# Performance work log

Measured on AMD Instinct MI355X. Metric: run time of the kernel, lower is better.

## Reference

```python
import jax, jax.numpy as jnp
import numpy as np

N_NODES = 50000
N_EDGES = 800000
D_IN = 128
D_HID = 256


def setup_inputs() -> dict:
    key = jax.random.key(0)
    ks = jax.random.split(key, 8)
    x = jax.random.normal(ks[0], (N_NODES, D_IN), dtype=jnp.float32)
    edge_index = jax.random.randint(ks[1], (2, N_EDGES), 0, N_NODES, dtype=jnp.int32)
    s1 = 1.0 / np.sqrt(D_IN)
    s2 = 1.0 / np.sqrt(D_HID)
    W1_l = jax.random.uniform(ks[2], (D_IN, D_HID), jnp.float32, -s1, s1)
    W1_r = jax.random.uniform(ks[3], (D_IN, D_HID), jnp.float32, -s1, s1)
    b1 = jax.random.uniform(ks[4], (D_HID,), jnp.float32, -s1, s1)
    W2_l = jax.random.uniform(ks[5], (D_HID, D_HID), jnp.float32, -s2, s2)
    W2_r = jax.random.uniform(ks[6], (D_HID, D_HID), jnp.float32, -s2, s2)
    b2 = jax.random.uniform(ks[7], (D_HID,), jnp.float32, -s2, s2)
    return {"x": x, "edge_index": edge_index,
            "W1_l": W1_l, "W1_r": W1_r, "b1": b1,
            "W2_l": W2_l, "W2_r": W2_r, "b2": b2}


def _sage_conv(x, src, dst, deg_inv, W_l, W_r, b):
    # mean-aggregate neighbor features at destination nodes, then
    # out = lin_l(mean_neighbors) + lin_r(x)  (PyG SAGEConv, mean aggr)
    msgs = x[src]                                              # [E, d]  irregular gather
    agg = jax.ops.segment_sum(msgs, dst, num_segments=x.shape[0])  # [N, d] scatter-add
    mean = agg * deg_inv[:, None]
    return mean @ W_l + x @ W_r + b


def reference(x, edge_index, W1_l, W1_r, b1, W2_l, W2_r, b2):
    src, dst = edge_index[0], edge_index[1]
    n = x.shape[0]
    deg = jax.ops.segment_sum(jnp.ones_like(dst, dtype=x.dtype), dst, num_segments=n)
    deg_inv = jnp.where(deg > 0, 1.0 / jnp.maximum(deg, 1.0), 0.0)
    h = jax.nn.relu(_sage_conv(x, src, dst, deg_inv, W1_l, W1_r, b1))
    # dropout is identity in eval mode
    out = jax.nn.relu(_sage_conv(h, src, dst, deg_inv, W2_l, W2_r, b2))
    return out
```

## Files before the change

kernel.cpp:

```cpp
#include <hip/hip_runtime.h>
#include <hip/hip_bf16.h>


#define DIN 128
#define DH  256
#define ELLW 64

typedef __attribute__((ext_vector_type(8))) short short8v;
typedef __attribute__((ext_vector_type(4))) float float4v;
typedef __attribute__((ext_vector_type(2))) float float2v;

__device__ __forceinline__ void gload_lds16(const void* g, void* l) {
    __builtin_amdgcn_global_load_lds((const __attribute__((address_space(1))) void*)g,
                                     (__attribute__((address_space(3))) void*)l, 16, 0, 0);
}
__device__ __forceinline__ float bf2f(unsigned short u) {
    union { unsigned int i; float f; } c; c.i = ((unsigned int)u) << 16; return c.f;
}
__device__ __forceinline__ unsigned short f2bf(float f) {
    union { float f; unsigned int i; } c; c.f = f;
    unsigned int lsb = (c.i >> 16) & 1u;
    return (unsigned short)((c.i + 0x7fffu + lsb) >> 16);
}
__device__ __host__ __forceinline__ int permcol(int q) {
    return ((q >> 6) << 6) + ((q & 3) << 4) + ((q >> 2) & 15);
}

__global__ void fill_ell(const int* __restrict__ src, const int* __restrict__ dst,
                         int* __restrict__ cnt, unsigned short* __restrict__ ell, int E) {
    int base = (blockIdx.x * blockDim.x + threadIdx.x) * 8;
    if (base + 7 < E) {
        int4 da = *(const int4*)(dst + base);
        int4 db = *(const int4*)(dst + base + 4);
        int4 sa = *(const int4*)(src + base);
        int4 sb = *(const int4*)(src + base + 4);
        int p0 = atomicAdd(&cnt[da.x], 1);
        int p1 = atomicAdd(&cnt[da.y], 1);
        int p2 = atomicAdd(&cnt[da.z], 1);
        int p3 = atomicAdd(&cnt[da.w], 1);
        int p4 = atomicAdd(&cnt[db.x], 1);
        int p5 = atomicAdd(&cnt[db.y], 1);
        int p6 = atomicAdd(&cnt[db.z], 1);
        int p7 = atomicAdd(&cnt[db.w], 1);
        if (p0 < ELLW) ell[(size_t)da.x * ELLW + p0] = (unsigned short)sa.x;
        if (p1 < ELLW) ell[(size_t)da.y * ELLW + p1] = (unsigned short)sa.y;
        if (p2 < ELLW) ell[(size_t)da.z * ELLW + p2] = (unsigned short)sa.z;
        if (p3 < ELLW) ell[(size_t)da.w * ELLW + p3] = (unsigned short)sa.w;
        if (p4 < ELLW) ell[(size_t)db.x * ELLW + p4] = (unsigned short)sb.x;
        if (p5 < ELLW) ell[(size_t)db.y * ELLW + p5] = (unsigned short)sb.y;
        if (p6 < ELLW) ell[(size_t)db.z * ELLW + p6] = (unsigned short)sb.z;
        if (p7 < ELLW) ell[(size_t)db.w * ELLW + p7] = (unsigned short)sb.w;
    } else {
        for (int e = base; e < E; ++e) {
            int d = dst[e];
            int p = atomicAdd(&cnt[d], 1);
            if (p < ELLW) ell[(size_t)d * ELLW + p] = (unsigned short)src[e];
        }
    }
}

__global__ void prep_weights(const float* __restrict__ W1l, const float* __restrict__ W1r,
                             const float* __restrict__ W2l, const float* __restrict__ W2r,
                             unsigned short* __restrict__ Wt1, unsigned short* __restrict__ Wt2) {
    int id = blockIdx.x * 256 + threadIdx.x;
    if (id < 256 * 256) {
        int n = id >> 8, k = id & 255;
        float v = (k < 128) ? W1l[k * 256 + n] : W1r[(k - 128) * 256 + n];
        Wt1[n * 256 + k] = f2bf(v);
    } else {
        int id2 = id - 256 * 256;
        if (id2 < 256 * 512) {
            int n = id2 >> 9, k = id2 & 511;
            float v;
            if (k < 256) v = W2l[permcol(k) * 256 + n];
            else         v = W2r[permcol(k - 256) * 256 + n];
            Wt2[n * 512 + k] = f2bf(v);
        }
    }
}

__global__ void conv_x(const float* __restrict__ x, unsigned short* __restrict__ Acat1,
                       unsigned char* __restrict__ xf8, int N) {
    int id = blockIdx.x * 256 + threadIdx.x;
    int base = id * 4;
    if (base < N * 128) {
        float4 v = *(const float4*)(x + base);
        int row = base >> 7, c = base & 127;
        ushort4 o;
        o.x = f2bf(v.x); o.y = f2bf(v.y); o.z = f2bf(v.z); o.w = f2bf(v.w);
        *(ushort4*)(Acat1 + (size_t)row * 256 + 128 + c) = o;
        int p = __builtin_amdgcn_cvt_pk_fp8_f32(v.x, v.y, 0, false);
        p = __builtin_amdgcn_cvt_pk_fp8_f32(v.z, v.w, p, true);
        *(unsigned int*)(xf8 + (size_t)row * 128 + c) = (unsigned int)p;
    }
}

template <int LANES, int RSTRB, int WSTR>
__global__ __launch_bounds__(256) void agg_fp8(const unsigned char* __restrict__ f8,
                                               const unsigned short* __restrict__ ell,
                                               const int* __restrict__ cnt,
                                               unsigned short* __restrict__ outp, int N) {
    int tid = threadIdx.x;
    constexpr int NPB = 256 / LANES;
    int node = blockIdx.x * NPB + tid / LANES;
    int lane = tid % LANES;
    if (node >= N) return;
    int cn = cnt[node];
    int dg = min(cn, ELLW);
    const unsigned short* row = ell + (size_t)node * ELLW;
    const unsigned char* fb = f8 + (size_t)lane * 16;
    float acc[16];
#pragma unroll
    for (int e = 0; e < 16; ++e) acc[e] = 0.f;
    int j = 0;
    for (; j + 8 <= dg; j += 8) {
        int s[8];
#pragma unroll
        for (int q = 0; q < 8; ++q) s[q] = row[j + q];
        int4 v[8];
#pragma unroll
        for (int q = 0; q < 8; ++q) v[q] = *(const int4*)(fb + (size_t)s[q] * RSTRB);
#pragma unroll
        for (int q = 0; q < 8; ++q) {
            int wv[4] = {v[q].x, v[q].y, v[q].z, v[q].w};
#pragma unroll
            for (int wI = 0; wI < 4; ++wI) {
                float2v lo = __builtin_amdgcn_cvt_pk_f32_fp8(wv[wI], false);
                float2v hi = __builtin_amdgcn_cvt_pk_f32_fp8(wv[wI], true);
                acc[wI * 4 + 0] += lo[0];
                acc[wI * 4 + 1] += lo[1];
                acc[wI * 4 + 2] += hi[0];
                acc[wI * 4 + 3] += hi[1];
            }
        }
    }
    for (; j < dg; ++j) {
        int s = row[j];
        int4 v = *(const int4*)(fb + (size_t)s * RSTRB);
        int wv[4] = {v.x, v.y, v.z, v.w};
#pragma unroll
        for (int wI = 0; wI < 4; ++wI) {
            float2v lo = __builtin_amdgcn_cvt_pk_f32_fp8(wv[wI], false);
            float2v hi = __builtin_amdgcn_cvt_pk_f32_fp8(wv[wI], true);
            acc[wI * 4 + 0] += lo[0];
            acc[wI * 4 + 1] += lo[1];
            acc[wI * 4 + 2] += hi[0];
            acc[wI * 4 + 3] += hi[1];
        }
    }
    float di = (cn > 0) ? 1.0f / (float)cn : 0.0f;
    short8v o0, o1;
#pragma unroll
    for (int e = 0; e < 8; ++e) {
        o0[e] = (short)f2bf(acc[e] * di);
        o1[e] = (short)f2bf(acc[8 + e] * di);
    }
    unsigned short* wp = outp + (size_t)node * WSTR + lane * 16;
    *(short8v*)wp = o0;
    *(short8v*)(wp + 8) = o1;
}

template <int OUT_BF16>
__global__ __launch_bounds__(512) void gemm_mfma(const unsigned short* __restrict__ A, int lda,
                                                 const unsigned short* __restrict__ Wt, int K,
                                                 const float* __restrict__ bias,
                                                 float* __restrict__ outF,
                                                 unsigned short* __restrict__ outB, int ldo,
                                                 unsigned char* __restrict__ outF8,
                                                 int M) {
    __shared__ __align__(16) char lds[49152];
    char* ldsA = lds;
    char* ldsB = lds + 16384;

    const int tid = threadIdx.x;
    const int lane = tid & 63;
    const int wid = tid >> 6;
    const int wm = wid >> 2, wn = wid & 3;
    const int m0 = blockIdx.x * 128;

    float4v acc[4][4];
#pragma unroll
    for (int i = 0; i < 4; ++i)
#pragma unroll
        for (int j = 0; j < 4; ++j) acc[i][j] = (float4v)(0.f);

    int rA[2], cA[2], rB[4], cB[4];
#pragma unroll
    for (int i = 0; i < 2; ++i) {
        int blin = i * 8192 + tid * 16;
        int bdat = blin ^ (((blin >> 7) & 7) << 4);
        rA[i] = min(m0 + (bdat >> 7), M - 1);
        cA[i] = (bdat & 127) >> 1;
    }
#pragma unroll
    for (int i = 0; i < 4; ++i) {
        int blin = i * 8192 + tid * 16;
        int bdat = blin ^ (((blin >> 7) & 7) << 4);
        rB[i] = bdat >> 7;
        cB[i] = (bdat & 127) >> 1;
    }

    for (int kc = 0; kc < K; kc += 64) {
#pragma unroll
        for (int i = 0; i < 2; ++i)
            gload_lds16(A + (size_t)rA[i] * lda + kc + cA[i],
                        ldsA + i * 8192 + wid * 1024);
#pragma unroll
        for (int i = 0; i < 4; ++i)
            gload_lds16(Wt + (size_t)rB[i] * K + kc + cB[i],
                        ldsB + i * 8192 + wid * 1024);
        __syncthreads();

#pragma unroll
        for (int ks = 0; ks < 2; ++ks) {
            short8v af[4], bf[4];
            int cbyte = (ks * 32 + ((lane >> 4) << 3)) * 2;
#pragma unroll
            for (int mi = 0; mi < 4; ++mi) {
                int r = wm * 64 + mi * 16 + (lane & 15);
                int bdat = (r << 7) + cbyte;
                int blin = bdat ^ (((r & 7)) << 4);
                af[mi] = *(const short8v*)(ldsA + blin);
            }
#pragma unroll
            for (int ni = 0; ni < 4; ++ni) {
                int r = wn * 64 + ni * 16 + (lane & 15);
                int bdat = (r << 7) + cbyte;
                int blin = bdat ^ (((r & 7)) << 4);
                bf[ni] = *(const short8v*)(ldsB + blin);
            }
#pragma unroll
            for (int mi = 0; mi < 4; ++mi)
#pragma unroll
                for (int ni = 0; ni < 4; ++ni)
                    acc[mi][ni] = __builtin_amdgcn_mfma_f32_16x16x32_bf16(
                        af[mi], bf[ni], acc[mi][ni], 0, 0, 0);
        }
        __syncthreads();
    }

    const int cl = lane & 15;
    const int rq = (lane >> 4) * 4;
    if (OUT_BF16) {
        const int pbase = (wn * 16 + cl) * 4;
        float bvn[4];
#pragma unroll
        for (int ni = 0; ni < 4; ++ni) bvn[ni] = bias[wn * 64 + ni * 16 + cl];
#pragma unroll
        for (int mi = 0; mi < 4; ++mi) {
#pragma unroll
            for (int j = 0; j < 4; ++j) {
                int gr = m0 + wm * 64 + mi * 16 + rq + j;
                if (gr < M) {
                    float v0 = fmaxf(acc[mi][0][j] + bvn[0], 0.f);
                    float v1 = fmaxf(acc[mi][1][j] + bvn[1], 0.f);
                    float v2 = fmaxf(acc[mi][2][j] + bvn[2], 0.f);
                    float v3 = fmaxf(acc[mi][3][j] + bvn[3], 0.f);
                    ushort4 hb;
                    hb.x = f2bf(v0); hb.y = f2bf(v1);
                    hb.z = f2bf(v2); hb.w = f2bf(v3);
                    *(ushort4*)(outB + (size_t)gr * ldo + pbase) = hb;
                    int pb = __builtin_amdgcn_cvt_pk_fp8_f32(v0, v1, 0, false);
                    pb = __builtin_amdgcn_cvt_pk_fp8_f32(v2, v3, pb, true);
                    *(unsigned int*)(outF8 + (size_t)gr * 256 + pbase) = (unsigned int)pb;
                }
            }
        }
    } else {
#pragma unroll
        for (int ni = 0; ni < 4; ++ni) {
            int gn = wn * 64 + ni * 16 + cl;
            float bv = bias[gn];
#pragma unroll
            for (int mi = 0; mi < 4; ++mi) {
#pragma unroll
                for (int j = 0; j < 4; ++j) {
                    int gr = m0 + wm * 64 + mi * 16 + rq + j;
                    if (gr < M)
                        outF[(size_t)gr * 256 + gn] =
                            fmaxf(acc[mi][ni][j] + bv, 0.f);
                }
            }
        }
    }
}

extern "C" void kernel_launch(void* const* d_in, const int* in_sizes, int n_in,
                              void* d_out, int out_size, void* d_ws, size_t ws_size,
                              hipStream_t stream) {
    const float* x   = (const float*)d_in[0];
    const int*   ei  = (const int*)d_in[1];
    const float* W1l = (const float*)d_in[2];
    const float* W1r = (const float*)d_in[3];
    const float* b1  = (const float*)d_in[4];
    const float* W2l = (const float*)d_in[5];
    const float* W2r = (const float*)d_in[6];
    const float* b2  = (const float*)d_in[7];
    float* out = (float*)d_out;

    int N = in_sizes[0] / DIN;
    int E = in_sizes[1] / 2;
    const int* srcI = ei;
    const int* dstI = ei + E;

    char* w = (char*)d_ws;
    auto alloc = [&](size_t bytes) -> char* {
        char* p = w;
        w += (bytes + 255) & ~(size_t)255;
        return p;
    };
    int* cnt = (int*)alloc((size_t)N * 4);
    unsigned short* ell = (unsigned short*)alloc((size_t)N * ELLW * 2);
    unsigned short* Acat1 = (unsigned short*)alloc((size_t)N * 256 * 2);
    unsigned short* Acat2 = (unsigned short*)alloc((size_t)N * 512 * 2);
    unsigned short* Wt1   = (unsigned short*)alloc((size_t)256 * 256 * 2);
    unsigned short* Wt2   = (unsigned short*)alloc((size_t)256 * 512 * 2);
    unsigned char*  hf8   = (unsigned char*)alloc((size_t)N * 256);
    unsigned char*  xf8   = (unsigned char*)Acat2;

    (void)hipMemsetAsync(cnt, 0, (size_t)N * 4, stream);
    fill_ell<<<(E / 8 + 255) / 256, 256, 0, stream>>>(srcI, dstI, cnt, ell, E);

    prep_weights<<<768, 256, 0, stream>>>(W1l, W1r, W2l, W2r, Wt1, Wt2);
    conv_x<<<(N * 128 / 4 + 255) / 256, 256, 0, stream>>>(x, Acat1, xf8, N);

    int gridM = (N + 127) / 128;

    agg_fp8<8, 128, 256><<<(N + 31) / 32, 256, 0, stream>>>(xf8, ell, cnt, Acat1, N);
    gemm_mfma<1><<<gridM, 512, 0, stream>>>(Acat1, 256, Wt1, 256, b1,
                                            nullptr, Acat2 + 256, 512, hf8, N);
    agg_fp8<16, 256, 512><<<(N + 15) / 16, 256, 0, stream>>>(hf8, ell, cnt, Acat2, N);
    gemm_mfma<0><<<gridM, 512, 0, stream>>>(Acat2, 512, Wt2, 512, b2,
                                            out, nullptr, 256, nullptr, N);
}
```

Measured before the change: 169.5 us.

## Build ELL adjacency via two-pass binning with LDS-local slot assignment

Replaces the single-pass ELL fill, which did one global atomic per edge on per-node counters and scattered 2-byte stores, with a two-pass scheme. Edges are first binned into 64-node groups, replicated 8 ways by block to spread atomic contention. A second kernel then assigns ELL slots with LDS atomics and writes each group's rows out with coalesced 16-byte stores. This adds an extra kernel launch and a round trip through a bins buffer. Bins are capped at 256 entries, which silently drops edges if a bin overflows, and the hard-coded NBIN of 782 ties the code to this node count.

```diff
diff --git a/kernel.cpp b/kernel.cpp
--- a/kernel.cpp
+++ b/kernel.cpp
@@ -5,6 +5,8 @@
 #define DIN 128
 #define DH  256
 #define ELLW 64
+#define NBIN 782
+#define BCAP 256
 
 typedef __attribute__((ext_vector_type(8))) short short8v;
 typedef __attribute__((ext_vector_type(4))) float float4v;
@@ -26,37 +28,68 @@
     return ((q >> 6) << 6) + ((q & 3) << 4) + ((q >> 2) & 15);
 }
 
-__global__ void fill_ell(const int* __restrict__ src, const int* __restrict__ dst,
-                         int* __restrict__ cnt, unsigned short* __restrict__ ell, int E) {
-    int base = (blockIdx.x * blockDim.x + threadIdx.x) * 8;
-    if (base + 7 < E) {
-        int4 da = *(const int4*)(dst + base);
-        int4 db = *(const int4*)(dst + base + 4);
-        int4 sa = *(const int4*)(src + base);
-        int4 sb = *(const int4*)(src + base + 4);
-        int p0 = atomicAdd(&cnt[da.x], 1);
-        int p1 = atomicAdd(&cnt[da.y], 1);
-        int p2 = atomicAdd(&cnt[da.z], 1);
-        int p3 = atomicAdd(&cnt[da.w], 1);
-        int p4 = atomicAdd(&cnt[db.x], 1);
-        int p5 = atomicAdd(&cnt[db.y], 1);
-        int p6 = atomicAdd(&cnt[db.z], 1);
-        int p7 = atomicAdd(&cnt[db.w], 1);
-        if (p0 < ELLW) ell[(size_t)da.x * ELLW + p0] = (unsigned short)sa.x;
-        if (p1 < ELLW) ell[(size_t)da.y * ELLW + p1] = (unsigned short)sa.y;
-        if (p2 < ELLW) ell[(size_t)da.z * ELLW + p2] = (unsigned short)sa.z;
-        if (p3 < ELLW) ell[(size_t)da.w * ELLW + p3] = (unsigned short)sa.w;
-        if (p4 < ELLW) ell[(size_t)db.x * ELLW + p4] = (unsigned short)sb.x;
-        if (p5 < ELLW) ell[(size_t)db.y * ELLW + p5] = (unsigned short)sb.y;
-        if (p6 < ELLW) ell[(size_t)db.z * ELLW + p6] = (unsigned short)sb.z;
-        if (p7 < ELLW) ell[(size_t)db.w * ELLW + p7] = (unsigned short)sb.w;
+__global__ void fill_bins(const int* __restrict__ src, const int* __restrict__ dst,
+                          int* __restrict__ gcnt, unsigned int* __restrict__ bins, int E) {
+    int t = blockIdx.x * blockDim.x + threadIdx.x;
+    int xc = blockIdx.x & 7;
+    int base = t * 4;
+    if (base + 3 < E) {
+        int4 d4 = *(const int4*)(dst + base);
+        int4 s4 = *(const int4*)(src + base);
+        int dd[4] = {d4.x, d4.y, d4.z, d4.w};
+        int ss[4] = {s4.x, s4.y, s4.z, s4.w};
+#pragma unroll
+        for (int q = 0; q < 4; ++q) {
+            int idx = xc * NBIN + (dd[q] >> 6);
+            int p = atomicAdd(&gcnt[idx], 1);
+            if (p < BCAP)
+                bins[((size_t)idx << 8) + p] =
+                    (unsigned int)((ss[q] << 6) | (dd[q] & 63));
+        }
     } else {
         for (int e = base; e < E; ++e) {
-            int d = dst[e];
-            int p = atomicAdd(&cnt[d], 1);
-            if (p < ELLW) ell[(size_t)d * ELLW + p] = (unsigned short)src[e];
-        }
-    }
+            int d = dst[e], s = src[e];
+            int idx = xc * NBIN + (d >> 6);
+            int p = atomicAdd(&gcnt[idx], 1);
+            if (p < BCAP)
+                bins[((size_t)idx << 8) + p] =
+                    (unsigned int)((s << 6) | (d & 63));
+        }
+    }
+}
+
+__global__ __launch_bounds__(256) void build_ell(const unsigned int* __restrict__ bins,
+                                                 const int* __restrict__ gcnt,
+                                                 unsigned short* __restrict__ ell,
+                                                 int* __restrict__ cnt, int N) {
+    __shared__ unsigned short lell[64 * ELLW];
+    __shared__ int lcnt[64];
+    int g = blockIdx.x;
+    int tid = threadIdx.x;
+    if (tid < 64) lcnt[tid] = 0;
+    __syncthreads();
+#pragma unroll 1
+    for (int c = 0; c < 8; ++c) {
+        int idx = c * NBIN + g;
+        int count = min(gcnt[idx], BCAP);
+        const unsigned int* bp = bins + ((size_t)idx << 8);
+        for (int i = tid; i < count; i += 256) {
+            unsigned int ent = bp[i];
+            int node = ent & 63;
+            int s = (int)(ent >> 6);
+            int slot = atomicAdd(&lcnt[node], 1);
+            if (slot < ELLW) lell[node * ELLW + slot] = (unsigned short)s;
+        }
+    }
+    __syncthreads();
+    int gbase = g * 64;
+    int nvalid = min(64, N - gbase);
+    for (int i = tid; i < nvalid * 8; i += 256) {
+        int node = i >> 3, part = i & 7;
+        *(uint4*)(ell + (size_t)(gbase + node) * ELLW + part * 8) =
+            *(const uint4*)(lell + node * ELLW + part * 8);
+    }
+    if (tid < nvalid) cnt[gbase + tid] = lcnt[tid];
 }
 
 __global__ void prep_weights(const float* __restrict__ W1l, const float* __restrict__ W1r,
@@ -310,6 +343,8 @@
         return p;
     };
     int* cnt = (int*)alloc((size_t)N * 4);
+    int* gcnt = (int*)alloc((size_t)8 * NBIN * 4);
+    unsigned int* bins = (unsigned int*)alloc((size_t)8 * NBIN * BCAP * 4);
     unsigned short* ell = (unsigned short*)alloc((size_t)N * ELLW * 2);
     unsigned short* Acat1 = (unsigned short*)alloc((size_t)N * 256 * 2);
     unsigned short* Acat2 = (unsigned short*)alloc((size_t)N * 512 * 2);
@@ -318,8 +353,9 @@
     unsigned char*  hf8   = (unsigned char*)alloc((size_t)N * 256);
     unsigned char*  xf8   = (unsigned char*)Acat2;
 
-    (void)hipMemsetAsync(cnt, 0, (size_t)N * 4, stream);
-    fill_ell<<<(E / 8 + 255) / 256, 256, 0, stream>>>(srcI, dstI, cnt, ell, E);
+    (void)hipMemsetAsync(gcnt, 0, (size_t)8 * NBIN * 4, stream);
+    fill_bins<<<(E / 4 + 255) / 256, 256, 0, stream>>>(srcI, dstI, gcnt, bins, E);
+    build_ell<<<NBIN, 256, 0, stream>>>(bins, gcnt, ell, cnt, N);
 
     prep_weights<<<768, 256, 0, stream>>>(W1l, W1r, W2l, W2r, Wt1, Wt2);
     conv_x<<<(N * 128 / 4 + 255) / 256, 256, 0, stream>>>(x, Acat1, xf8, N);
```

Result: slower. 183.9 us (+8.5%).

## Partition ELL fill by destination-node groups matched to XCD index

Applied to the files above, without the earlier changes.

The ELL build kernel now runs a fixed grid of 2048 blocks. Each block takes the XCD slot blockIdx&7 and processes only the edges whose destination falls in the matching 64-node group (dst>>6)&7. Because blocks are dispatched round-robin across the eight XCDs, the atomics and ELL writes for a given destination should stay within one XCD's L2, avoiding cross-die coherence traffic. In exchange, every edge is read eight times, once per slot group, and the scheme depends on how the hardware assigns blocks to XCDs.

```diff
diff --git a/kernel.cpp b/kernel.cpp
--- a/kernel.cpp
+++ b/kernel.cpp
@@ -26,33 +26,34 @@
     return ((q >> 6) << 6) + ((q & 3) << 4) + ((q >> 2) & 15);
 }
 
-__global__ void fill_ell(const int* __restrict__ src, const int* __restrict__ dst,
-                         int* __restrict__ cnt, unsigned short* __restrict__ ell, int E) {
-    int base = (blockIdx.x * blockDim.x + threadIdx.x) * 8;
-    if (base + 7 < E) {
-        int4 da = *(const int4*)(dst + base);
-        int4 db = *(const int4*)(dst + base + 4);
-        int4 sa = *(const int4*)(src + base);
-        int4 sb = *(const int4*)(src + base + 4);
-        int p0 = atomicAdd(&cnt[da.x], 1);
-        int p1 = atomicAdd(&cnt[da.y], 1);
-        int p2 = atomicAdd(&cnt[da.z], 1);
-        int p3 = atomicAdd(&cnt[da.w], 1);
-        int p4 = atomicAdd(&cnt[db.x], 1);
-        int p5 = atomicAdd(&cnt[db.y], 1);
-        int p6 = atomicAdd(&cnt[db.z], 1);
-        int p7 = atomicAdd(&cnt[db.w], 1);
-        if (p0 < ELLW) ell[(size_t)da.x * ELLW + p0] = (unsigned short)sa.x;
-        if (p1 < ELLW) ell[(size_t)da.y * ELLW + p1] = (unsigned short)sa.y;
-        if (p2 < ELLW) ell[(size_t)da.z * ELLW + p2] = (unsigned short)sa.z;
-        if (p3 < ELLW) ell[(size_t)da.w * ELLW + p3] = (unsigned short)sa.w;
-        if (p4 < ELLW) ell[(size_t)db.x * ELLW + p4] = (unsigned short)sb.x;
-        if (p5 < ELLW) ell[(size_t)db.y * ELLW + p5] = (unsigned short)sb.y;
-        if (p6 < ELLW) ell[(size_t)db.z * ELLW + p6] = (unsigned short)sb.z;
-        if (p7 < ELLW) ell[(size_t)db.w * ELLW + p7] = (unsigned short)sb.w;
-    } else {
-        for (int e = base; e < E; ++e) {
-            int d = dst[e];
+__global__ __launch_bounds__(256) void fill_ell(const int* __restrict__ src,
+                                                const int* __restrict__ dst,
+                                                int* __restrict__ cnt,
+                                                unsigned short* __restrict__ ell, int E) {
+    int xc = blockIdx.x & 7;
+    int bslot = blockIdx.x >> 3;
+    int nslot = gridDim.x >> 3;
+    int per = (((E + nslot - 1) / nslot) + 3) & ~3;
+    int lo = bslot * per;
+    int hi = min(lo + per, E);
+    for (int base = lo + threadIdx.x * 4; base + 3 < hi; base += 256 * 4) {
+        int4 d4 = *(const int4*)(dst + base);
+        int4 s4 = *(const int4*)(src + base);
+        int dd[4] = {d4.x, d4.y, d4.z, d4.w};
+        int ss[4] = {s4.x, s4.y, s4.z, s4.w};
+#pragma unroll
+        for (int q = 0; q < 4; ++q) {
+            if (((dd[q] >> 6) & 7) == xc) {
+                int p = atomicAdd(&cnt[dd[q]], 1);
+                if (p < ELLW) ell[(size_t)dd[q] * ELLW + p] = (unsigned short)ss[q];
+            }
+        }
+    }
+    int tail = lo + ((hi - lo) & ~3);
+    if (threadIdx.x < (hi - tail)) {
+        int e = tail + threadIdx.x;
+        int d = dst[e];
+        if (((d >> 6) & 7) == xc) {
             int p = atomicAdd(&cnt[d], 1);
             if (p < ELLW) ell[(size_t)d * ELLW + p] = (unsigned short)src[e];
         }
@@ -319,7 +320,7 @@
     unsigned char*  xf8   = (unsigned char*)Acat2;
 
     (void)hipMemsetAsync(cnt, 0, (size_t)N * 4, stream);
-    fill_ell<<<(E / 8 + 255) / 256, 256, 0, stream>>>(srcI, dstI, cnt, ell, E);
+    fill_ell<<<2048, 256, 0, stream>>>(srcI, dstI, cnt, ell, E);
 
     prep_weights<<<768, 256, 0, stream>>>(W1l, W1r, W2l, W2r, Wt1, Wt2);
     conv_x<<<(N * 128 / 4 + 255) / 256, 256, 0, stream>>>(x, Acat1, xf8, N);
```

After: 169.6 us. Within noise of the previous version (+0.0%).
